# Kernel tuning notes

Measured on AMD Instinct MI355X. Metric: run time of the kernel, lower is better.

Reference implementation:

```python
import jax, jax.numpy as jnp
import numpy as np

NB, NC, IN, HID, OUT, ENG = 8, 16384, 64, 128, 64, 128
SYNC, DEBATE = 0.15, 0.15


def setup_inputs() -> dict:
    key = jax.random.key(0)
    ks = jax.random.split(key, 24)
    rn = lambda k, s, sc=0.05: jax.random.normal(k, s, jnp.float32) * sc
    return {
        "x": jax.random.normal(ks[0], (1, IN), jnp.float32),
        "noise": jax.random.normal(ks[1], (NB, 1, IN), jnp.float32),
        "amps": jax.random.uniform(ks[2], (NB,), jnp.float32, 0.5, 1.5),
        "hiddens": jax.random.normal(ks[3], (NB, NC, HID), jnp.float32) * 0.1,
        "eaW1": rn(ks[4], (ENG, IN + HID)), "eaB1": rn(ks[5], (ENG,)),
        "eaW2": rn(ks[6], (OUT, ENG)), "eaB2": rn(ks[7], (OUT,)),
        "egW1": rn(ks[8], (ENG, IN + HID)), "egB1": rn(ks[9], (ENG,)),
        "egW2": rn(ks[10], (OUT, ENG)), "egB2": rn(ks[11], (OUT,)),
        "gru_Wih": rn(ks[12], (3 * HID, OUT + 1)), "gru_Whh": rn(ks[13], (3 * HID, HID)),
        "gru_bih": rn(ks[14], (3 * HID,)), "gru_bhh": rn(ks[15], (3 * HID,)),
        "headW": rn(ks[16], (IN, OUT)), "headb": rn(ks[17], (IN,)),
        "mixW": rn(ks[18], (HID, HID * NB)), "mixb": rn(ks[19], (HID,)),
        "step": 10,
    }


def reference(x, noise, amps, hiddens, eaW1, eaB1, eaW2, eaB2,
              egW1, egB1, egW2, egB2, gru_Wih, gru_Whh, gru_bih, gru_bhh,
              headW, headb, mixW, mixb, step):
    sg = jax.lax.stop_gradient
    # per-branch perturbed input, broadcast over cells
    scale = 0.05 * jnp.arange(1, NB + 1, dtype=x.dtype)[:, None, None]
    xb = jnp.broadcast_to(x[None] + noise * scale, (NB, NC, IN))
    comb = jnp.concatenate([xb, hiddens], axis=-1)          # (NB,NC,IN+HID)
    a = jax.nn.relu(comb @ eaW1.T + eaB1) @ eaW2.T + eaB2
    g = jax.nn.relu(comb @ egW1.T + egB1) @ egW2.T + egB2
    out = a - g                                             # (NB,NC,OUT)
    tension = jnp.mean(out ** 2, axis=-1)                   # (NB,NC)

    # GRUCell update (mem input is detached in the original)
    mem_in = sg(jnp.concatenate([out, tension[..., None]], axis=-1))
    gi = mem_in @ gru_Wih.T + gru_bih                       # (NB,NC,3H)
    gh = hiddens @ gru_Whh.T + gru_bhh
    ir, iz, inn = jnp.split(gi, 3, axis=-1)
    hr, hz, hn = jnp.split(gh, 3, axis=-1)
    r = jax.nn.sigmoid(ir + hr)
    z = jax.nn.sigmoid(iz + hz)
    n = jnp.tanh(inn + r * hn)
    newh = sg((1.0 - z) * n + z * hiddens)                  # stored detached

    # faction sync + debate (state only)
    nf = min(8, NC // 2)
    fs = NC // nf
    core = newh[:, :nf * fs].reshape(NB, nf, fs, HID)
    core = (1.0 - SYNC) * core + SYNC * core.mean(axis=2, keepdims=True)
    if step > 5:
        glob = core.mean(axis=2).mean(axis=1)               # (NB,HID)
        dc = max(1, fs // 4)
        core = core.at[:, :, :dc].set(
            (1.0 - DEBATE) * core[:, :, :dc] + DEBATE * glob[:, None, None, :])
    newh = jnp.concatenate([core.reshape(NB, nf * fs, HID), newh[:, nf * fs:]], axis=1)

    # amplitude-weighted branch combine (amps used via .item() -> constants)
    aabs = jnp.abs(amps)
    aabs = aabs / (aabs.sum() + 1e-8)
    cell_out = jnp.einsum('b,bnd->nd', sg(aabs), out)       # (NC,OUT)
    avg_t = tension.mean(axis=0)                            # (NC,)
    w = jax.nn.softmax(sg(avg_t))                           # weights from .item()'d tensions
    combined = (w[:, None] * cell_out).sum(axis=0, keepdims=True)  # (1,OUT)
    pred = combined @ headW.T + headb                       # (1,IN)

    # interference mixer state update on branch 0
    interf = newh.mean(axis=1).reshape(1, -1) @ mixW.T + mixb       # (1,HID)
    newh = newh.at[0].add(sg(interf) * 0.05)

    return pred, avg_t.mean(), newh
```

## Files before the change

### kernel.cpp

```cpp
#include <hip/hip_runtime.h>
#include <math.h>

#define NB   8
#define NCC  16384
#define HID  128

typedef __attribute__((ext_vector_type(8))) short short8;
typedef __attribute__((ext_vector_type(4))) float f32x4;

#define MFMA(a,b,c) __builtin_amdgcn_mfma_f32_16x16x32_bf16(a,b,c,0,0,0)

#define WS_AABS   0
#define WS_BASE1  8
#define WS_BOUT   2056
#define WS_BSUMR  2120
#define WS_BSUMZ  2248
#define WS_BIHN   2376
#define WS_BHHN   2504
#define WS_W64    2632
#define WS_INTERF 3024
#define WS_FRAG   3152
#define WS_SD     64592
#define WS_AVGT   73808
#define WS_TS     90192
#define WS_FMEAN  221264
#define WS_PART2  230480
#define WS_FPART  246864
#define WS_CO     771152
#define WS_PARTE  1819728
#define WS_PARTA  1819984

__device__ __forceinline__ unsigned short f2b(float f) {
    unsigned int u = __float_as_uint(f);
    unsigned int r = (u + 0x7fffu + ((u >> 16) & 1u)) >> 16;
    return (unsigned short)r;
}
__device__ __forceinline__ float b2f(unsigned short us) {
    return __uint_as_float(((unsigned int)us) << 16);
}
__device__ __forceinline__ float sigm(float x) {
    return __builtin_amdgcn_rcpf(1.f + __expf(-x));
}
__device__ __forceinline__ float tanh_fast(float x) {
    return 1.f - 2.f * __builtin_amdgcn_rcpf(__expf(2.f * x) + 1.f);
}
__device__ __forceinline__ unsigned int cvtpk(float lo, float hi) {
    unsigned int r;
    asm volatile("v_cvt_pk_bf16_f32 %0, %1, %2" : "=v"(r) : "v"(lo), "v"(hi));
    return r;
}
__device__ __forceinline__ void stg(char* dst, int row, int cb, float4 u, float4 v) {
    uint4 pk = make_uint4(cvtpk(u.x, u.y), cvtpk(u.z, u.w),
                          cvtpk(v.x, v.y), cvtpk(v.z, v.w));
    *(uint4*)(dst + row * 256 + (cb ^ ((row & 7) << 4))) = pk;
}

__global__ __launch_bounds__(1024) void kprep(
    const float* __restrict__ x, const float* __restrict__ noise,
    const float* __restrict__ amps,
    const float* __restrict__ eaW1, const float* __restrict__ eaB1,
    const float* __restrict__ egW1, const float* __restrict__ egB1,
    const float* __restrict__ eaW2, const float* __restrict__ eaB2,
    const float* __restrict__ egW2, const float* __restrict__ egB2,
    const float* __restrict__ gWih, const float* __restrict__ gWhh,
    const float* __restrict__ gbih, const float* __restrict__ gbhh,
    float* __restrict__ ws)
{
    int i = blockIdx.x * 1024 + threadIdx.x;
    if (i < 122880) {
        short* wsh = (short*)(ws + WS_FRAG);
        float v;
        if (i < 32768) {
            int rel = i;
            int j = rel & 7, l = (rel >> 3) & 63, tk = rel >> 9;
            int kt = tk & 3, nt = tk >> 2;
            int n = nt * 16 + (l & 15), k = kt * 32 + ((l >> 4) << 3) + j;
            v = (n < 128) ? eaW1[n * 192 + 64 + k] : egW1[(n - 128) * 192 + 64 + k];
        } else if (i < 49152) {
            int rel = i - 32768;
            int j = rel & 7, l = (rel >> 3) & 63, tk = rel >> 9;
            int kt = tk & 7, nt = tk >> 3;
            int d = nt * 16 + (l & 15), k = kt * 32 + ((l >> 4) << 3) + j;
            v = (k < 128) ? eaW2[d * 128 + k] : -egW2[d * 128 + (k - 128)];
        } else if (i < 73728) {
            int rel = i - 49152;
            int j = rel & 7, l = (rel >> 3) & 63, tk = rel >> 9;
            int kt = tk & 1, nt = tk >> 1;
            int r = nt * 16 + (l & 15), k = kt * 32 + ((l >> 4) << 3) + j;
            v = gWih[r * 65 + k];
        } else {
            int rel = i - 73728;
            int j = rel & 7, l = (rel >> 3) & 63, tk = rel >> 9;
            int kt = tk & 3, nt = tk >> 2;
            int r = nt * 16 + (l & 15), k = kt * 32 + ((l >> 4) << 3) + j;
            v = gWhh[r * 128 + k];
        }
        wsh[i] = (short)f2b(v);
    }
    if (blockIdx.x == 0) {
        __shared__ float xb[8][64];
        int t = threadIdx.x;
        if (t < 512) {
            int b = t >> 6, k = t & 63;
            xb[b][k] = x[k] + noise[b * 64 + k] * (0.05f * (float)(b + 1));
        }
        if (t == 0) {
            float s = 0.f;
            for (int b = 0; b < 8; b++) s += fabsf(amps[b]);
            s += 1e-8f;
            for (int b = 0; b < 8; b++) ws[WS_AABS + b] = fabsf(amps[b]) / s;
        }
        __syncthreads();
        for (int ii = t; ii < 2048; ii += 1024) {
            int b = ii >> 8, n = ii & 255;
            const float* Wp; float s;
            if (n < 128) { Wp = eaW1 + n * 192; s = eaB1[n]; }
            else         { Wp = egW1 + (n - 128) * 192; s = egB1[n - 128]; }
            for (int k = 0; k < 64; k++) s += xb[b & 7][k] * Wp[k];
            ws[WS_BASE1 + ii] = s;
        }
        if (t < 64) ws[WS_BOUT + t] = eaB2[t] - egB2[t];
        if (t < 128) {
            ws[WS_BSUMR + t] = gbih[t] + gbhh[t];
            ws[WS_BSUMZ + t] = gbih[128 + t] + gbhh[128 + t];
            ws[WS_BIHN + t]  = gbih[256 + t];
            ws[WS_BHHN + t]  = gbhh[256 + t];
        }
        if (t < 384) ws[WS_W64 + t] = gWih[t * 65 + 64];
    }
}

__global__ __launch_bounds__(1024) void kA(
    const float* __restrict__ hiddens, float* __restrict__ newh,
    float* __restrict__ ws)
{
    __shared__ char  wlds[98304];
    __shared__ char  hsb[64 * 256];
    __shared__ char  agb[64 * 512];
    __shared__ float ts_s[64];
    __shared__ float tsum_s[64];

    const int t    = threadIdx.x;
    const int lane = t & 63;
    const int w    = t >> 6;
    const int rg   = w >> 2;
    const int nq   = w & 3;
    const int col  = lane & 15;
    const int kq   = lane >> 4;
    const int r0   = rg * 16;
    const int n0   = blockIdx.x * 64;

    {
        const float4* src = (const float4*)(ws + WS_FRAG);
        float4* dst = (float4*)wlds;
#pragma unroll
        for (int p = 0; p < 6; p++) dst[p * 1024 + t] = src[p * 1024 + t];
    }
    const short8* W1F = (const short8*)wlds;
    const short8* W2F = (const short8*)(wlds + 65536);

    const float bo = ws[WS_BOUT + nq * 16 + col];
    float co_reg[4];
#pragma unroll
    for (int i = 0; i < 4; i++) co_reg[i] = 0.f;
    if (t < 64) tsum_s[t] = 0.f;

    const int flat = t * 8;
    const int srow = flat >> 7;
    const int scb  = (flat & 127) * 2;

    {
        const float* hs = hiddens + (size_t)n0 * HID;
        float4 a0 = *(const float4*)(hs + flat);
        float4 a1 = *(const float4*)(hs + flat + 4);
        stg(hsb, srow, scb, a0, a1);
    }
    float4 pfa0, pfa1;
    unsigned short* outu = (unsigned short*)newh;

    for (int b = 0; b < NB; ++b) {
        __syncthreads();
        if (t < 64) {
            if (b > 0) {
                ws[WS_TS + (size_t)(b - 1) * NCC + n0 + t] = ts_s[t];
                tsum_s[t] += ts_s[t];
            }
            ts_s[t] = 0.f;
        }
        if (b < 7) {
            const float* hsn = hiddens + ((size_t)((b + 1) * NCC + n0)) * HID;
            pfa0 = *(const float4*)(hsn + flat);
            pfa1 = *(const float4*)(hsn + flat + 4);
        }

        {
            short8 aH[4];
#pragma unroll
            for (int ks = 0; ks < 4; ks++) {
                int row = r0 + col;
                aH[ks] = *(const short8*)(hsb + row * 256 +
                           ((ks * 64 + (kq << 4)) ^ ((row & 7) << 4)));
            }
#pragma unroll
            for (int nti = 0; nti < 4; nti++) {
                int nt = nq * 4 + nti;
                f32x4 ac = {0.f, 0.f, 0.f, 0.f};
#pragma unroll
                for (int kt = 0; kt < 4; kt++)
                    ac = MFMA(aH[kt], W1F[(nt * 4 + kt) * 64 + lane], ac);
                int n = nt * 16 + col;
                float bs = ws[WS_BASE1 + b * 256 + n];
#pragma unroll
                for (int j = 0; j < 4; j++) {
                    int row = r0 + (kq << 2) + j;
                    float v = fmaxf(ac[j] + bs, 0.f);
                    *(unsigned short*)(agb + row * 512 +
                        ((n * 2) ^ ((row & 7) << 4))) = f2b(v);
                }
            }
        }
        __syncthreads();

        if (b < 7) stg(hsb, srow, scb, pfa0, pfa1);

        {
            f32x4 ov = {0.f, 0.f, 0.f, 0.f};
#pragma unroll
            for (int kt = 0; kt < 8; kt++) {
                int kb = kt * 64 + (kq << 4);
                int ra = r0 + col;
                short8 a0 = *(const short8*)(agb + ra * 512 + (kb ^ ((ra & 7) << 4)));
                ov = MFMA(a0, W2F[(nq * 8 + kt) * 64 + lane], ov);
            }
            int d = nq * 16 + col;
            float aab = ws[WS_AABS + b];
#pragma unroll
            for (int j = 0; j < 4; j++) {
                int row = r0 + (kq << 2) + j;
                float v = ov[j] + bo;
                co_reg[j] += aab * v;
                outu[(size_t)(b * NCC + n0 + row) * 256 + 192 + d] = f2b(v);
                float sq = v * v;
                sq += __shfl_xor(sq, 1);
                sq += __shfl_xor(sq, 2);
                sq += __shfl_xor(sq, 4);
                sq += __shfl_xor(sq, 8);
                if (col == 0) atomicAdd(&ts_s[row], sq);
            }
        }
    }
    __syncthreads();
    if (t < 64) {
        ws[WS_TS + (size_t)7 * NCC + n0 + t] = ts_s[t];
        tsum_s[t] += ts_s[t];
        ws[WS_AVGT + n0 + t] = tsum_s[t] * (1.f / 512.f);
    }
    {
        int d = nq * 16 + col;
#pragma unroll
        for (int j = 0; j < 4; j++) {
            int row = r0 + (kq << 2) + j;
            ws[WS_CO + (size_t)(n0 + row) * 64 + d] = co_reg[j];
        }
    }
}

__global__ __launch_bounds__(1024) void kB(
    const float* __restrict__ hiddens, float* __restrict__ newh,
    float* __restrict__ ws)
{
    __shared__ char  wl[147456];
    __shared__ char  hsb[32 * 256];
    __shared__ char  otb[32 * 128];
    __shared__ float ts_s[32];
    __shared__ float fp2[2][128];

    const int t    = threadIdx.x;
    const int lane = t & 63;
    const int w    = t >> 6;
    const int rh   = w >> 3;
    const int hg   = w & 7;
    const int col  = lane & 15;
    const int kq   = lane >> 4;
    const int chunk = blockIdx.x;
    const int n0   = chunk * 32;

    {
        const float4* src = (const float4*)(ws + WS_FRAG) + 6144;
        float4* dst = (float4*)wl;
#pragma unroll
        for (int p = 0; p < 9; p++) dst[p * 1024 + t] = src[p * 1024 + t];
    }
    const short8* WIHF = (const short8*)wl;
    const short8* WHHF = (const short8*)(wl + 49152);
    const unsigned short* outu = (const unsigned short*)newh;

    const int h = hg * 16 + col;
    const float bsr = ws[WS_BSUMR + h];
    const float bsz = ws[WS_BSUMZ + h];
    const float bin = ws[WS_BIHN + h];
    const float bhn = ws[WS_BHHN + h];
    const float wr  = ws[WS_W64 + h];
    const float wz  = ws[WS_W64 + 128 + h];
    const float wn  = ws[WS_W64 + 256 + h];

    const int flat = t * 8;
    const int srow = flat >> 7;
    const int scb  = (flat & 127) * 2;
    const int ocell = t >> 4;
    const int ooff  = (t & 15) * 4;

    float4 rh0 = {0,0,0,0}, rh1 = {0,0,0,0};
    uint2  ro = make_uint2(0, 0);
    float  rts = 0.f;
    if (t < 512) {
        const float* hs = hiddens + (size_t)n0 * HID;
        rh0 = *(const float4*)(hs + flat);
        rh1 = *(const float4*)(hs + flat + 4);
        ro  = *(const uint2*)(outu + (size_t)(n0 + ocell) * 256 + 192 + ooff);
    }
    if (t < 32) rts = ws[WS_TS + n0 + t];

    for (int b = 0; b < NB; ++b) {
        if (t < 512) {
            stg(hsb, srow, scb, rh0, rh1);
            *(uint2*)(otb + ocell * 128 + ((ooff * 2) ^ ((ocell & 7) << 4))) = ro;
        }
        if (t < 32) ts_s[t] = rts;
        __syncthreads();

        if (b < 7) {
            if (t < 512) {
                const float* hsn = hiddens + ((size_t)((b + 1) * NCC + n0)) * HID;
                rh0 = *(const float4*)(hsn + flat);
                rh1 = *(const float4*)(hsn + flat + 4);
                ro  = *(const uint2*)(outu + (size_t)((b + 1) * NCC + n0 + ocell) * 256 + 192 + ooff);
            }
            if (t < 32) rts = ws[WS_TS + (size_t)(b + 1) * NCC + n0 + t];
        }

        {
            float* nbase = newh + ((size_t)(b * NCC + n0)) * HID;
            const int ra = rh * 16 + col;
            f32x4 R = {0.f,0.f,0.f,0.f};
            f32x4 Z = {0.f,0.f,0.f,0.f};
            f32x4 I = {0.f,0.f,0.f,0.f};
            f32x4 N = {0.f,0.f,0.f,0.f};
#pragma unroll
            for (int ks = 0; ks < 2; ks++) {
                short8 a0 = *(const short8*)(otb + ra * 128 +
                             ((ks * 64 + (kq << 4)) ^ ((ra & 7) << 4)));
                R = MFMA(a0, WIHF[(hg * 2 + ks) * 64 + lane], R);
                Z = MFMA(a0, WIHF[((hg + 8) * 2 + ks) * 64 + lane], Z);
                I = MFMA(a0, WIHF[((hg + 16) * 2 + ks) * 64 + lane], I);
            }
#pragma unroll
            for (int ks = 0; ks < 4; ks++) {
                short8 a0 = *(const short8*)(hsb + ra * 256 +
                             ((ks * 64 + (kq << 4)) ^ ((ra & 7) << 4)));
                R = MFMA(a0, WHHF[(hg * 4 + ks) * 64 + lane], R);
                Z = MFMA(a0, WHHF[((hg + 8) * 4 + ks) * 64 + lane], Z);
                N = MFMA(a0, WHHF[((hg + 16) * 4 + ks) * 64 + lane], N);
            }
            float flsum = 0.f;
#pragma unroll
            for (int j = 0; j < 4; j++) {
                int row = rh * 16 + (kq << 2) + j;
                float tv = ts_s[row] * (1.f / 64.f);
                float r  = sigm(R[j] + bsr + tv * wr);
                float z  = sigm(Z[j] + bsz + tv * wz);
                float hn = N[j] + bhn;
                float nn = tanh_fast(I[j] + bin + tv * wn + r * hn);
                float hold = b2f(*(const unsigned short*)(hsb + row * 256 +
                                 ((h * 2) ^ ((row & 7) << 4))));
                float nh = (1.f - z) * nn + z * hold;
                nbase[(size_t)row * HID + h] = nh;
                flsum += nh;
            }
            flsum += __shfl_xor(flsum, 16);
            flsum += __shfl_xor(flsum, 32);
            if (kq == 0) fp2[rh][h] = flsum;
        }
        __syncthreads();

        if (t < 128)
            ws[WS_FPART + ((size_t)(b * 512 + chunk)) * 128 + t] = fp2[0][t] + fp2[1][t];
    }
}

__global__ __launch_bounds__(256) void kfr(float* __restrict__ ws)
{
    int blk = blockIdx.x, t = threadIdx.x;
    if (blk < 256) {
        __shared__ float wexp[64];
        __shared__ float red[256];
        int n0 = blk * 64;
        float av = 0.f;
        if (t < 64) {
            av = ws[WS_AVGT + n0 + t];
            wexp[t] = __expf(av);
        }
        __syncthreads();
        int d = t & 63, q = t >> 6;
        float s = 0.f;
        for (int i = 0; i < 16; i++) {
            int c = q * 16 + i;
            s += wexp[c] * ws[WS_CO + (size_t)(n0 + c) * 64 + d];
        }
        red[t] = s; __syncthreads();
        if (t < 64)
            ws[WS_PART2 + blk * 64 + t] = red[t] + red[64 + t] + red[128 + t] + red[192 + t];
        if (t < 64) {
            float e = wexp[t], a2 = av;
            e  += __shfl_xor(e, 1);  a2 += __shfl_xor(a2, 1);
            e  += __shfl_xor(e, 2);  a2 += __shfl_xor(a2, 2);
            e  += __shfl_xor(e, 4);  a2 += __shfl_xor(a2, 4);
            e  += __shfl_xor(e, 8);  a2 += __shfl_xor(a2, 8);
            e  += __shfl_xor(e, 16); a2 += __shfl_xor(a2, 16);
            e  += __shfl_xor(e, 32); a2 += __shfl_xor(a2, 32);
            if (t == 0) { ws[WS_PARTE + blk] = e; ws[WS_PARTA + blk] = a2; }
        }
    } else {
        int bf = blk - 256;
        int b = bf >> 3, f = bf & 7;
        if (t < 128) {
            int h = t;
            float s = 0.f, s8 = 0.f;
            for (int j = 0; j < 64; j++) {
                float v = ws[WS_FPART + ((size_t)(b * 512 + f * 64 + j)) * 128 + h];
                s += v;
                if (j < 16) s8 += v;
            }
            ws[WS_FMEAN + (b * 8 + f) * 128 + h] = s * (1.f / 2048.f);
            ws[WS_SD + (b * 8 + f) * 128 + h] = s8;
        }
    }
}

__global__ __launch_bounds__(256) void kmp(
    const float* __restrict__ mixW, const float* __restrict__ mixb,
    const float* __restrict__ headW, const float* __restrict__ headb,
    const int* __restrict__ step, float* __restrict__ ws,
    float* __restrict__ d_out)
{
    int blk = blockIdx.x, t = threadIdx.x;
    if (blk < 128) {
        __shared__ float hm[1024];
        __shared__ float red[256];
        bool deb = (step[0] > 5);
        for (int j = t; j < 1024; j += 256) {
            int b = j >> 7, hh = j & 127;
            float s = 0.f, sd = 0.f;
            for (int f = 0; f < 8; f++) {
                s  += ws[WS_FMEAN + (b * 8 + f) * 128 + hh];
                sd += ws[WS_SD + (b * 8 + f) * 128 + hh];
            }
            float gl = s * 0.125f;
            float tot = 16384.f * gl;
            if (deb) tot += 0.15f * (3481.6f * gl - 0.85f * sd);
            hm[j] = tot * (1.f / 16384.f);
        }
        __syncthreads();
        float4 wv = *(const float4*)(mixW + (size_t)blk * 1024 + t * 4);
        float4 hv = *(const float4*)(&hm[t * 4]);
        float s = wv.x * hv.x + wv.y * hv.y + wv.z * hv.z + wv.w * hv.w;
        red[t] = s; __syncthreads();
        for (int st = 128; st > 0; st >>= 1) { if (t < st) red[t] += red[t + st]; __syncthreads(); }
        if (t == 0) ws[WS_INTERF + blk] = mixb[blk] + red[0];
    } else {
        __shared__ float red[256];
        __shared__ float num[64];
        __shared__ float den_s;
        int d = t & 63, q = t >> 6;
        float s = 0.f;
        for (int i = 0; i < 64; i++) s += ws[WS_PART2 + (q * 64 + i) * 64 + d];
        red[t] = s; __syncthreads();
        if (t < 64) num[t] = red[t] + red[64 + t] + red[128 + t] + red[192 + t];
        __syncthreads();
        red[t] = ws[WS_PARTE + t]; __syncthreads();
        for (int st = 128; st > 0; st >>= 1) { if (t < st) red[t] += red[t + st]; __syncthreads(); }
        if (t == 0) den_s = red[0];
        __syncthreads();
        red[t] = ws[WS_PARTA + t]; __syncthreads();
        for (int st = 128; st > 0; st >>= 1) { if (t < st) red[t] += red[t + st]; __syncthreads(); }
        if (t == 0) d_out[64] = red[0] * (1.f / (float)NCC);
        __syncthreads();
        if (t < 64) {
            float inv_den = 1.f / den_s;
            float p = headb[t];
            for (int d2 = 0; d2 < 64; d2++) p += (num[d2] * inv_den) * headW[t * 64 + d2];
            d_out[t] = p;
        }
    }
}

__global__ __launch_bounds__(256) void k35_blend(
    float* __restrict__ newh, const float* __restrict__ ws,
    const int* __restrict__ step)
{
    int blk = blockIdx.x;
    int b = blk >> 8, ck = blk & 255;
    int t = threadIdx.x;
    int h4 = t & 31;
    int cg = t >> 5;
    int base = ck * 64;
    int f = base >> 11;
    bool deb = (step[0] > 5) && ((base & 2047) < 512);
    float4 fm = *(const float4*)(ws + WS_FMEAN + (size_t)(b * 8 + f) * 128 + h4 * 4);
    float glx = 0.f, gly = 0.f, glz = 0.f, glw = 0.f;
    for (int ff = 0; ff < 8; ff++) {
        float4 v = *(const float4*)(ws + WS_FMEAN + (size_t)(b * 8 + ff) * 128 + h4 * 4);
        glx += v.x; gly += v.y; glz += v.z; glw += v.w;
    }
    glx *= 0.125f; gly *= 0.125f; glz *= 0.125f; glw *= 0.125f;
    float4 itf = {0.f, 0.f, 0.f, 0.f};
    if (b == 0) {
        float4 iv = *(const float4*)(ws + WS_INTERF + h4 * 4);
        itf.x = 0.05f * iv.x; itf.y = 0.05f * iv.y;
        itf.z = 0.05f * iv.z; itf.w = 0.05f * iv.w;
    }
    for (int i = 0; i < 8; i++) {
        int cell = base + i * 8 + cg;
        size_t idx = ((size_t)b * NCC + cell) * 128 + h4 * 4;
        float4 v = *(float4*)(newh + idx);
        v.x = 0.85f * v.x + 0.15f * fm.x;
        v.y = 0.85f * v.y + 0.15f * fm.y;
        v.z = 0.85f * v.z + 0.15f * fm.z;
        v.w = 0.85f * v.w + 0.15f * fm.w;
        if (deb) {
            v.x = 0.85f * v.x + 0.15f * glx;
            v.y = 0.85f * v.y + 0.15f * gly;
            v.z = 0.85f * v.z + 0.15f * glz;
            v.w = 0.85f * v.w + 0.15f * glw;
        }
        v.x += itf.x; v.y += itf.y; v.z += itf.z; v.w += itf.w;
        *(float4*)(newh + idx) = v;
    }
}

extern "C" void kernel_launch(void* const* d_in, const int* in_sizes, int n_in,
                              void* d_out, int out_size, void* d_ws, size_t ws_size,
                              hipStream_t stream)
{
    const float* x       = (const float*)d_in[0];
    const float* noise   = (const float*)d_in[1];
    const float* amps    = (const float*)d_in[2];
    const float* hiddens = (const float*)d_in[3];
    const float* eaW1    = (const float*)d_in[4];
    const float* eaB1    = (const float*)d_in[5];
    const float* eaW2    = (const float*)d_in[6];
    const float* eaB2    = (const float*)d_in[7];
    const float* egW1    = (const float*)d_in[8];
    const float* egB1    = (const float*)d_in[9];
    const float* egW2    = (const float*)d_in[10];
    const float* egB2    = (const float*)d_in[11];
    const float* gWih    = (const float*)d_in[12];
    const float* gWhh    = (const float*)d_in[13];
    const float* gbih    = (const float*)d_in[14];
    const float* gbhh    = (const float*)d_in[15];
    const float* headW   = (const float*)d_in[16];
    const float* headb   = (const float*)d_in[17];
    const float* mixW    = (const float*)d_in[18];
    const float* mixb    = (const float*)d_in[19];
    const int*   step    = (const int*)d_in[20];

    float* out  = (float*)d_out;
    float* newh = out + 65;
    float* ws   = (float*)d_ws;

    kprep<<<120, 1024, 0, stream>>>(x, noise, amps, eaW1, eaB1, egW1, egB1,
                                    eaW2, eaB2, egW2, egB2, gWih, gWhh,
                                    gbih, gbhh, ws);
    kA<<<256, 1024, 0, stream>>>(hiddens, newh, ws);
    kB<<<512, 1024, 0, stream>>>(hiddens, newh, ws);
    kfr<<<320, 256, 0, stream>>>(ws);
    kmp<<<129, 256, 0, stream>>>(mixW, mixb, headW, headb, step, ws, out);
    k35_blend<<<2048, 256, 0, stream>>>(newh, ws, step);
}
```

Before: 124.6 us.

## Double GRU kernel tile to 64 cells and keep input weights in registers

The GRU update kernel now handles 64 cells per block instead of 32, so every thread takes part in staging and each wave computes two 16-row MFMA subtiles. The input-to-hidden weight fragments move out of shared memory into registers, loaded once from global memory, which shrinks the shared weight copy from 144KB to 96KB. This halves the block count and the per-block weight staging, and the reduction kernel is changed to match the new partial-sum layout. The cost is more registers per thread and fewer blocks to spread over the CUs.

```diff
diff --git a/kernel.cpp b/kernel.cpp
--- a/kernel.cpp
+++ b/kernel.cpp
@@ -269,31 +269,39 @@
     const float* __restrict__ hiddens, float* __restrict__ newh,
     float* __restrict__ ws)
 {
-    __shared__ char  wl[147456];
-    __shared__ char  hsb[32 * 256];
-    __shared__ char  otb[32 * 128];
-    __shared__ float ts_s[32];
+    __shared__ char  wl[98304];
+    __shared__ char  hsb[64 * 256];
+    __shared__ char  otb[64 * 128];
+    __shared__ float ts_s[64];
     __shared__ float fp2[2][128];
 
     const int t    = threadIdx.x;
     const int lane = t & 63;
     const int w    = t >> 6;
-    const int rh   = w >> 3;
+    const int rg   = w >> 3;
     const int hg   = w & 7;
     const int col  = lane & 15;
     const int kq   = lane >> 4;
     const int chunk = blockIdx.x;
-    const int n0   = chunk * 32;
+    const int n0   = chunk * 64;
 
     {
-        const float4* src = (const float4*)(ws + WS_FRAG) + 6144;
+        const float4* src = (const float4*)(ws + WS_FRAG) + 9216;
         float4* dst = (float4*)wl;
 #pragma unroll
-        for (int p = 0; p < 9; p++) dst[p * 1024 + t] = src[p * 1024 + t];
-    }
-    const short8* WIHF = (const short8*)wl;
-    const short8* WHHF = (const short8*)(wl + 49152);
+        for (int p = 0; p < 6; p++) dst[p * 1024 + t] = src[p * 1024 + t];
+    }
+    const short8* WHHF = (const short8*)wl;
     const unsigned short* outu = (const unsigned short*)newh;
+
+    const short8* WIHG = (const short8*)((const short*)(ws + WS_FRAG) + 49152);
+    short8 wihR[2], wihZ[2], wihI[2];
+#pragma unroll
+    for (int ks = 0; ks < 2; ks++) {
+        wihR[ks] = WIHG[(hg * 2 + ks) * 64 + lane];
+        wihZ[ks] = WIHG[((hg + 8) * 2 + ks) * 64 + lane];
+        wihI[ks] = WIHG[((hg + 16) * 2 + ks) * 64 + lane];
+    }
 
     const int h = hg * 16 + col;
     const float bsr = ws[WS_BSUMR + h];
@@ -310,81 +318,81 @@
     const int ocell = t >> 4;
     const int ooff  = (t & 15) * 4;
 
-    float4 rh0 = {0,0,0,0}, rh1 = {0,0,0,0};
-    uint2  ro = make_uint2(0, 0);
+    float4 rh0, rh1;
+    uint2  ro;
     float  rts = 0.f;
-    if (t < 512) {
+    {
         const float* hs = hiddens + (size_t)n0 * HID;
         rh0 = *(const float4*)(hs + flat);
         rh1 = *(const float4*)(hs + flat + 4);
         ro  = *(const uint2*)(outu + (size_t)(n0 + ocell) * 256 + 192 + ooff);
     }
-    if (t < 32) rts = ws[WS_TS + n0 + t];
+    if (t < 64) rts = ws[WS_TS + n0 + t];
 
     for (int b = 0; b < NB; ++b) {
-        if (t < 512) {
-            stg(hsb, srow, scb, rh0, rh1);
-            *(uint2*)(otb + ocell * 128 + ((ooff * 2) ^ ((ocell & 7) << 4))) = ro;
-        }
-        if (t < 32) ts_s[t] = rts;
+        stg(hsb, srow, scb, rh0, rh1);
+        *(uint2*)(otb + ocell * 128 + ((ooff * 2) ^ ((ocell & 7) << 4))) = ro;
+        if (t < 64) ts_s[t] = rts;
         __syncthreads();
 
         if (b < 7) {
-            if (t < 512) {
-                const float* hsn = hiddens + ((size_t)((b + 1) * NCC + n0)) * HID;
-                rh0 = *(const float4*)(hsn + flat);
-                rh1 = *(const float4*)(hsn + flat + 4);
-                ro  = *(const uint2*)(outu + (size_t)((b + 1) * NCC + n0 + ocell) * 256 + 192 + ooff);
-            }
-            if (t < 32) rts = ws[WS_TS + (size_t)(b + 1) * NCC + n0 + t];
+            const float* hsn = hiddens + ((size_t)((b + 1) * NCC + n0)) * HID;
+            rh0 = *(const float4*)(hsn + flat);
+            rh1 = *(const float4*)(hsn + flat + 4);
+            ro  = *(const uint2*)(outu + (size_t)((b + 1) * NCC + n0 + ocell) * 256 + 192 + ooff);
+            if (t < 64) rts = ws[WS_TS + (size_t)(b + 1) * NCC + n0 + t];
         }
 
         {
             float* nbase = newh + ((size_t)(b * NCC + n0)) * HID;
-            const int ra = rh * 16 + col;
-            f32x4 R = {0.f,0.f,0.f,0.f};
-            f32x4 Z = {0.f,0.f,0.f,0.f};
-            f32x4 I = {0.f,0.f,0.f,0.f};
-            f32x4 N = {0.f,0.f,0.f,0.f};
-#pragma unroll
-            for (int ks = 0; ks < 2; ks++) {
-                short8 a0 = *(const short8*)(otb + ra * 128 +
-                             ((ks * 64 + (kq << 4)) ^ ((ra & 7) << 4)));
-                R = MFMA(a0, WIHF[(hg * 2 + ks) * 64 + lane], R);
-                Z = MFMA(a0, WIHF[((hg + 8) * 2 + ks) * 64 + lane], Z);
-                I = MFMA(a0, WIHF[((hg + 16) * 2 + ks) * 64 + lane], I);
-            }
-#pragma unroll
-            for (int ks = 0; ks < 4; ks++) {
-                short8 a0 = *(const short8*)(hsb + ra * 256 +
-                             ((ks * 64 + (kq << 4)) ^ ((ra & 7) << 4)));
-                R = MFMA(a0, WHHF[(hg * 4 + ks) * 64 + lane], R);
-                Z = MFMA(a0, WHHF[((hg + 8) * 4 + ks) * 64 + lane], Z);
-                N = MFMA(a0, WHHF[((hg + 16) * 4 + ks) * 64 + lane], N);
-            }
             float flsum = 0.f;
 #pragma unroll
-            for (int j = 0; j < 4; j++) {
-                int row = rh * 16 + (kq << 2) + j;
-                float tv = ts_s[row] * (1.f / 64.f);
-                float r  = sigm(R[j] + bsr + tv * wr);
-                float z  = sigm(Z[j] + bsz + tv * wz);
-                float hn = N[j] + bhn;
-                float nn = tanh_fast(I[j] + bin + tv * wn + r * hn);
-                float hold = b2f(*(const unsigned short*)(hsb + row * 256 +
-                                 ((h * 2) ^ ((row & 7) << 4))));
-                float nh = (1.f - z) * nn + z * hold;
-                nbase[(size_t)row * HID + h] = nh;
-                flsum += nh;
+            for (int st = 0; st < 2; ++st) {
+                const int rbase = rg * 32 + st * 16;
+                const int ra = rbase + col;
+                f32x4 R = {0.f,0.f,0.f,0.f};
+                f32x4 Z = {0.f,0.f,0.f,0.f};
+                f32x4 I = {0.f,0.f,0.f,0.f};
+                f32x4 N = {0.f,0.f,0.f,0.f};
+#pragma unroll
+                for (int ks = 0; ks < 2; ks++) {
+                    short8 a0 = *(const short8*)(otb + ra * 128 +
+                                 ((ks * 64 + (kq << 4)) ^ ((ra & 7) << 4)));
+                    R = MFMA(a0, wihR[ks], R);
+                    Z = MFMA(a0, wihZ[ks], Z);
+                    I = MFMA(a0, wihI[ks], I);
+                }
+#pragma unroll
+                for (int ks = 0; ks < 4; ks++) {
+                    short8 a0 = *(const short8*)(hsb + ra * 256 +
+                                 ((ks * 64 + (kq << 4)) ^ ((ra & 7) << 4)));
+                    R = MFMA(a0, WHHF[(hg * 4 + ks) * 64 + lane], R);
+                    Z = MFMA(a0, WHHF[((hg + 8) * 4 + ks) * 64 + lane], Z);
+                    N = MFMA(a0, WHHF[((hg + 16) * 4 + ks) * 64 + lane], N);
+                }
+#pragma unroll
+                for (int j = 0; j < 4; j++) {
+                    int row = rbase + (kq << 2) + j;
+                    float tv = ts_s[row] * (1.f / 64.f);
+                    float r  = sigm(R[j] + bsr + tv * wr);
+                    float z  = sigm(Z[j] + bsz + tv * wz);
+                    float hn = N[j] + bhn;
+                    float nn = tanh_fast(I[j] + bin + tv * wn + r * hn);
+                    float hold = b2f(*(const unsigned short*)(hsb + row * 256 +
+                                     ((h * 2) ^ ((row & 7) << 4))));
+                    float nh = (1.f - z) * nn + z * hold;
+                    nbase[(size_t)row * HID + h] = nh;
+                    flsum += nh;
+                }
             }
             flsum += __shfl_xor(flsum, 16);
             flsum += __shfl_xor(flsum, 32);
-            if (kq == 0) fp2[rh][h] = flsum;
+            if (kq == 0) fp2[rg][h] = flsum;
         }
         __syncthreads();
 
         if (t < 128)
-            ws[WS_FPART + ((size_t)(b * 512 + chunk)) * 128 + t] = fp2[0][t] + fp2[1][t];
+            ws[WS_FPART + ((size_t)(b * 256 + chunk)) * 128 + t] = fp2[0][t] + fp2[1][t];
     }
 }
 
@@ -426,10 +434,10 @@
         if (t < 128) {
             int h = t;
             float s = 0.f, s8 = 0.f;
-            for (int j = 0; j < 64; j++) {
-                float v = ws[WS_FPART + ((size_t)(b * 512 + f * 64 + j)) * 128 + h];
+            for (int j = 0; j < 32; j++) {
+                float v = ws[WS_FPART + ((size_t)(b * 256 + f * 32 + j)) * 128 + h];
                 s += v;
-                if (j < 16) s8 += v;
+                if (j < 8) s8 += v;
             }
             ws[WS_FMEAN + (b * 8 + f) * 128 + h] = s * (1.f / 2048.f);
             ws[WS_SD + (b * 8 + f) * 128 + h] = s8;
@@ -572,7 +580,7 @@
                                     eaW2, eaB2, egW2, egB2, gWih, gWhh,
                                     gbih, gbhh, ws);
     kA<<<256, 1024, 0, stream>>>(hiddens, newh, ws);
-    kB<<<512, 1024, 0, stream>>>(hiddens, newh, ws);
+    kB<<<256, 1024, 0, stream>>>(hiddens, newh, ws);
     kfr<<<320, 256, 0, stream>>>(ws);
     kmp<<<129, 256, 0, stream>>>(mixW, mixb, headW, headb, step, ws, out);
     k35_blend<<<2048, 256, 0, stream>>>(newh, ws, step);
```

After: 119.3 us. 4.3% less time.
